# Kernel optimization log

Measured on AMD Instinct MI355X. Metric: run time of the kernel, lower is better.

Reference implementation:

```python
import jax, jax.numpy as jnp
import numpy as np
from jax import lax

B, T, D, U = 128, 1024, 256, 48


def setup_inputs() -> dict:
    key = jax.random.key(0)
    k1, k2, k3 = jax.random.split(key, 3)
    x = jax.random.normal(k1, (B, T, D), dtype=jnp.float32)
    kernel = jax.random.normal(k2, (D, U), dtype=jnp.float32) * (1.0 / np.sqrt(D))
    bias = jnp.zeros((U,), dtype=jnp.float32)
    chain_kernel = jax.random.normal(k3, (U, U), dtype=jnp.float32)
    return {"x": x, "kernel": kernel, "bias": bias, "chain_kernel": chain_kernel}


def _viterbi_decode(logits, trans):
    # logits: [B, T, U], trans: [U, U]; full-length sequences (mask=None)
    init_state = logits[:, 0]  # [B, U]
    steps = jnp.swapaxes(logits[:, 1:], 0, 1)  # [T-1, B, U]

    def fwd(state, logit_t):
        # scores[b, i, j] = state[b, i] + trans[i, j]
        scores = state[:, :, None] + trans[None]  # [B, U, U]
        bp = jnp.argmax(scores, axis=1)            # [B, U] best prev tag
        new_state = logit_t + jnp.max(scores, axis=1)
        return new_state, bp

    final_state, bps = lax.scan(fwd, init_state, steps)  # bps: [T-1, B, U]
    last_tag = jnp.argmax(final_state, axis=-1)          # [B]

    def back(tag, bp):
        prev = jnp.take_along_axis(bp, tag[:, None], axis=1)[:, 0]
        return prev, prev

    # reverse scan emits tags for t = 0..T-2 in forward time order
    _, tags_head = lax.scan(back, last_tag, bps, reverse=True)  # [T-1, B]
    tags = jnp.concatenate([tags_head, last_tag[None]], axis=0)  # [T, B]
    return jnp.transpose(tags)  # [B, T]


def reference(x, kernel, bias, chain_kernel):
    # _dense_layer: linear activation -> x @ kernel + bias
    logits = jnp.einsum('btd,du->btu', x, kernel) + bias  # [B, T, U]
    pred_ids = _viterbi_decode(logits, chain_kernel)       # [B, T] int
    return pred_ids.astype(jnp.float32)
```

## Files before the change

kernel.cpp:

```cpp
#include <hip/hip_runtime.h>
#include <cstdint>

#define B_ 128
#define T_ 1024
#define D_ 256
#define U_ 48

__device__ __forceinline__ float max3f(float a, float b, float c) {
    float d;
    asm("v_max3_f32 %0, %1, %2, %3" : "=v"(d) : "v"(a), "v"(b), "v"(c));
    return d;
}

__global__ __launch_bounds__(256, 1) void k_logits(const float* __restrict__ x,
                                                   const float* __restrict__ kern,
                                                   const float* __restrict__ bias,
                                                   float* __restrict__ logits) {
    __shared__ float K[D_ * U_];
    __shared__ float bsh[U_];
    const int tid = threadIdx.x;
    for (int i = tid; i < D_ * U_; i += 256) K[i] = kern[i];
    if (tid < U_) bsh[tid] = bias[tid];
    __syncthreads();

    const long row0 = (long)blockIdx.x * 256 + tid;
    const long row1 = row0 + (long)B_ * T_ / 2;
    const float4* xr0 = (const float4*)(x + row0 * D_);
    const float4* xr1 = (const float4*)(x + row1 * D_);

    float a0[U_], a1[U_];
#pragma unroll
    for (int u = 0; u < U_; ++u) { a0[u] = 0.0f; a1[u] = 0.0f; }

#pragma unroll 1
    for (int blk = 0; blk < D_ / 32; ++blk) {
        float4 xa[8], xb[8];
#pragma unroll
        for (int i = 0; i < 8; ++i) xa[i] = xr0[blk * 8 + i];
#pragma unroll
        for (int i = 0; i < 8; ++i) xb[i] = xr1[blk * 8 + i];

#pragma unroll
        for (int i = 0; i < 8; ++i) {
            const int d4 = blk * 8 + i;
            const float xc0[4] = {xa[i].x, xa[i].y, xa[i].z, xa[i].w};
            const float xc1[4] = {xb[i].x, xb[i].y, xb[i].z, xb[i].w};
#pragma unroll
            for (int c = 0; c < 4; ++c) {
                const float4* kp = (const float4*)&K[(d4 * 4 + c) * U_];
                const float s0 = xc0[c], s1 = xc1[c];
#pragma unroll
                for (int u4 = 0; u4 < U_ / 4; ++u4) {
                    float4 kv = kp[u4];
                    a0[u4*4+0] += s0 * kv.x;  a1[u4*4+0] += s1 * kv.x;
                    a0[u4*4+1] += s0 * kv.y;  a1[u4*4+1] += s1 * kv.y;
                    a0[u4*4+2] += s0 * kv.z;  a1[u4*4+2] += s1 * kv.z;
                    a0[u4*4+3] += s0 * kv.w;  a1[u4*4+3] += s1 * kv.w;
                }
            }
        }
    }

    float4* o0 = (float4*)(logits + row0 * U_);
    float4* o1 = (float4*)(logits + row1 * U_);
#pragma unroll
    for (int i = 0; i < U_ / 4; ++i) {
        float4 v0, v1;
        v0.x = a0[i*4+0] + bsh[i*4+0];  v1.x = a1[i*4+0] + bsh[i*4+0];
        v0.y = a0[i*4+1] + bsh[i*4+1];  v1.y = a1[i*4+1] + bsh[i*4+1];
        v0.z = a0[i*4+2] + bsh[i*4+2];  v1.z = a1[i*4+2] + bsh[i*4+2];
        v0.w = a0[i*4+3] + bsh[i*4+3];  v1.w = a1[i*4+3] + bsh[i*4+3];
        o0[i] = v0;
        o1[i] = v1;
    }
}

__device__ __forceinline__ float maxplus_rlb(float state, const float* tc) {
    const int si = __float_as_int(state);
    int sv[U_];
#pragma unroll
    for (int v = 0; v < U_; ++v) sv[v] = __builtin_amdgcn_readlane(si, v);
    __builtin_amdgcn_sched_barrier(0);
    float cf[U_];
#pragma unroll
    for (int v = 0; v < U_; ++v) cf[v] = __int_as_float(sv[v]) + tc[v];
    float t1[16];
#pragma unroll
    for (int i = 0; i < 16; ++i) t1[i] = max3f(cf[3*i], cf[3*i+1], cf[3*i+2]);
    float t2[6];
#pragma unroll
    for (int i = 0; i < 5; ++i) t2[i] = max3f(t1[3*i], t1[3*i+1], t1[3*i+2]);
    t2[5] = t1[15];
    return fmaxf(max3f(t2[0], t2[1], t2[2]), max3f(t2[3], t2[4], t2[5]));
}

__global__ __launch_bounds__(64, 1) void k_forward(const float* __restrict__ trans,
                                                   const float* __restrict__ logits,
                                                   float* __restrict__ delta) {
    const int lane = threadIdx.x;
    const int b = blockIdx.x;
    const int u = (lane < U_) ? lane : (U_ - 1);

    float tc[U_];
#pragma unroll
    for (int v = 0; v < U_; ++v) tc[v] = trans[v * U_ + u];

    const float* lin = logits + (long)b * T_ * U_;
    float* dout = delta + (long)b * T_ * U_;

    float state = lin[u];
    dout[u] = state;

    float pf[8];
#pragma unroll
    for (int i = 0; i < 8; ++i) pf[i] = lin[(1 + i) * U_ + u];

    const float* lp = lin + 9 * U_ + u;
    float* dp = dout + 1 * U_ + u;

#pragma unroll 1
    for (int g = 0; g < 127; ++g) {
#pragma unroll
        for (int j = 0; j < 8; ++j) {
            const float logit = pf[j];
            pf[j] = lp[j * U_];
            const float m = maxplus_rlb(state, tc);
            state = logit + m;
            dp[j * U_] = state;
        }
        lp += 8 * U_;
        dp += 8 * U_;
    }

#pragma unroll
    for (int j = 0; j < 7; ++j) {
        const float m = maxplus_rlb(state, tc);
        state = pf[j] + m;
        dp[j * U_] = state;
    }
}

__global__ __launch_bounds__(64, 1) void k_forward_inplace(const float* __restrict__ trans,
                                                           float* __restrict__ delta) {
    const int lane = threadIdx.x;
    const int b = blockIdx.x;
    const int u = (lane < U_) ? lane : (U_ - 1);

    float tc[U_];
#pragma unroll
    for (int v = 0; v < U_; ++v) tc[v] = trans[v * U_ + u];

    float* base = delta + (long)b * T_ * U_;
    float state = base[u];

#pragma unroll 1
    for (int t = 1; t < T_; ++t) {
        const float logit = base[(long)t * U_ + u];
        const float m = maxplus_rlb(state, tc);
        state = logit + m;
        base[(long)t * U_ + u] = state;
    }
}

#define BP_ROWS 32
__global__ __launch_bounds__(64, 1) void k_bp(const float* __restrict__ trans,
                                              const float* __restrict__ delta,
                                              unsigned char* __restrict__ bp) {
    __shared__ float sbuf[2][U_];
    const int lane = threadIdx.x;
    const int u = (lane < U_) ? lane : (U_ - 1);

    float tc[U_];
#pragma unroll
    for (int v = 0; v < U_; ++v) tc[v] = trans[v * U_ + u];

    const int NROW = B_ * (T_ - 1);
    const int row0 = blockIdx.x * BP_ROWS;
    if (row0 >= NROW) return;

    int b = row0 / (T_ - 1);
    int tm1 = row0 - b * (T_ - 1);

    float dval = delta[((long)b * T_ + tm1) * U_ + u];

#pragma unroll 1
    for (int i = 0; i < BP_ROWS; ++i) {
        const int row = row0 + i;
        if (row >= NROW) break;

        sbuf[i & 1][u] = dval;

        int bn = b, tn = tm1 + 1;
        if (tn == T_ - 1) { tn = 0; bn = b + 1; }
        float dnext = 0.0f;
        if (row + 1 < NROW) dnext = delta[((long)bn * T_ + tn) * U_ + u];

        const float4* sb4 = (const float4*)sbuf[i & 1];
        float best = -3.4e38f;
        int bi = 0;
#pragma unroll
        for (int k = 0; k < U_ / 4; ++k) {
            float4 s = sb4[k];
            float c0 = s.x + tc[4*k+0];
            float c1 = s.y + tc[4*k+1];
            float c2 = s.z + tc[4*k+2];
            float c3 = s.w + tc[4*k+3];
            bi = (c0 > best) ? 4*k+0 : bi;  best = fmaxf(best, c0);
            bi = (c1 > best) ? 4*k+1 : bi;  best = fmaxf(best, c1);
            bi = (c2 > best) ? 4*k+2 : bi;  best = fmaxf(best, c2);
            bi = (c3 > best) ? 4*k+3 : bi;  best = fmaxf(best, c3);
        }
        bp[(long)row * U_ + u] = (unsigned char)bi;

        b = bn; tm1 = tn; dval = dnext;
    }
}

__global__ __launch_bounds__(64) void k_back(const float* __restrict__ delta,
                                             const unsigned char* __restrict__ bp,
                                             float* __restrict__ out) {
    __shared__ unsigned char bpl[(T_ - 1) * U_];
    __shared__ float tags[T_];
    __shared__ float fin[U_];
    const int lane = threadIdx.x;
    const int b = blockIdx.x;

    const uint32_t* src = (const uint32_t*)(bp + (long)b * (T_ - 1) * U_);
    uint32_t* dst = (uint32_t*)bpl;
    const int NW = (T_ - 1) * U_ / 4;
    for (int i = lane; i < NW; i += 64) dst[i] = src[i];
    if (lane < U_) fin[lane] = delta[((long)b * T_ + (T_ - 1)) * U_ + lane];
    __syncthreads();

    if (lane == 0) {
        float best = fin[0];
        int tag = 0;
        for (int uu = 1; uu < U_; ++uu)
            if (fin[uu] > best) { best = fin[uu]; tag = uu; }
        tags[T_ - 1] = (float)tag;
        for (int t = T_ - 1; t >= 1; --t) {
            tag = bpl[(t - 1) * U_ + tag];
            tags[t - 1] = (float)tag;
        }
    }
    __syncthreads();

    float* o = out + (long)b * T_;
    for (int i = lane; i < T_; i += 64) o[i] = tags[i];
}

extern "C" void kernel_launch(void* const* d_in, const int* in_sizes, int n_in,
                              void* d_out, int out_size, void* d_ws, size_t ws_size,
                              hipStream_t stream) {
    const float* x     = (const float*)d_in[0];
    const float* kern  = (const float*)d_in[1];
    const float* bias  = (const float*)d_in[2];
    const float* trans = (const float*)d_in[3];
    float* out = (float*)d_out;

    const size_t NBT = (size_t)B_ * T_ * U_ * sizeof(float);

    float* logits = (float*)d_ws;
    const bool two_buf = ws_size >= 2 * NBT + (size_t)B_ * T_ * U_;
    float* delta = two_buf ? (float*)((char*)d_ws + NBT) : logits;
    unsigned char* bp = (unsigned char*)d_ws + (two_buf ? 2 * NBT : NBT);

    const int NROW = B_ * (T_ - 1);
    const int bp_grid = (NROW + BP_ROWS - 1) / BP_ROWS;

    k_logits<<<(B_ * T_ / 2) / 256, 256, 0, stream>>>(x, kern, bias, logits);
    if (two_buf)
        k_forward<<<B_, 64, 0, stream>>>(trans, logits, delta);
    else
        k_forward_inplace<<<B_, 64, 0, stream>>>(trans, logits);
    k_bp  <<<bp_grid, 64, 0, stream>>>(trans, delta, bp);
    k_back<<<B_,      64, 0, stream>>>(delta, bp, out);
}
```

Baseline: 565.9 us.

## Replace readlane broadcast with DPP wave rotation in Viterbi max-plus step

```diff
diff --git a/kernel.cpp b/kernel.cpp
--- a/kernel.cpp
+++ b/kernel.cpp
@@ -10,6 +10,10 @@
     float d;
     asm("v_max3_f32 %0, %1, %2, %3" : "=v"(d) : "v"(a), "v"(b), "v"(c));
     return d;
+}
+
+__device__ __forceinline__ float ror1f(float x) {
+    return __int_as_float(__builtin_amdgcn_mov_dpp(__float_as_int(x), 0x13C, 0xF, 0xF, true));
 }
 
 __global__ __launch_bounds__(256, 1) void k_logits(const float* __restrict__ x,
@@ -75,23 +79,45 @@
     }
 }
 
-__device__ __forceinline__ float maxplus_rlb(float state, const float* tc) {
-    const int si = __float_as_int(state);
-    int sv[U_];
-#pragma unroll
-    for (int v = 0; v < U_; ++v) sv[v] = __builtin_amdgcn_readlane(si, v);
-    __builtin_amdgcn_sched_barrier(0);
-    float cf[U_];
-#pragma unroll
-    for (int v = 0; v < U_; ++v) cf[v] = __int_as_float(sv[v]) + tc[v];
-    float t1[16];
-#pragma unroll
-    for (int i = 0; i < 16; ++i) t1[i] = max3f(cf[3*i], cf[3*i+1], cf[3*i+2]);
-    float t2[6];
-#pragma unroll
-    for (int i = 0; i < 5; ++i) t2[i] = max3f(t1[3*i], t1[3*i+1], t1[3*i+2]);
-    t2[5] = t1[15];
-    return fmaxf(max3f(t2[0], t2[1], t2[2]), max3f(t2[3], t2[4], t2[5]));
+__device__ __forceinline__ float maxplus_dpp(float state, const float* tr,
+                                             int lane, int baddr) {
+    const float rsrc = (lane < U_) ? state : -3.0e38f;
+    const int rbi = __builtin_amdgcn_ds_bpermute(baddr, __float_as_int(rsrc));
+
+    float rA = rsrc;
+    float c0 = rA + tr[0];
+    rA = ror1f(rA);
+    float c1 = rA + tr[1];
+    float m = fmaxf(c0, c1);
+#pragma unroll
+    for (int k = 2; k < 32; k += 2) {
+        rA = ror1f(rA); float ca = rA + tr[k];
+        rA = ror1f(rA); float cb = rA + tr[k + 1];
+        m = max3f(m, ca, cb);
+    }
+    float rB = __int_as_float(rbi);
+    float d0 = rB + tr[32];
+    rB = ror1f(rB);
+    float d1 = rB + tr[33];
+    m = max3f(m, d0, d1);
+#pragma unroll
+    for (int k = 34; k < 64; k += 2) {
+        rB = ror1f(rB); float ca = rB + tr[k];
+        rB = ror1f(rB); float cb = rB + tr[k + 1];
+        m = max3f(m, ca, cb);
+    }
+    return m;
+}
+
+__device__ __forceinline__ void load_tr(const float* __restrict__ trans,
+                                        float* tr, int lane, int u) {
+    const int p = __builtin_amdgcn_mov_dpp(lane, 0x13C, 0xF, 0xF, true);
+    const int dirm = (p - lane) & 63;
+#pragma unroll
+    for (int k = 0; k < 64; ++k) {
+        const int w = (lane + dirm * k) & 63;
+        tr[k] = (w < U_) ? trans[w * U_ + u] : 0.0f;
+    }
 }
 
 __global__ __launch_bounds__(64, 1) void k_forward(const float* __restrict__ trans,
@@ -100,16 +126,16 @@
     const int lane = threadIdx.x;
     const int b = blockIdx.x;
     const int u = (lane < U_) ? lane : (U_ - 1);
-
-    float tc[U_];
-#pragma unroll
-    for (int v = 0; v < U_; ++v) tc[v] = trans[v * U_ + u];
+    const int baddr = ((lane + 32) & 63) * 4;
+
+    float tr[64];
+    load_tr(trans, tr, lane, u);
 
     const float* lin = logits + (long)b * T_ * U_;
     float* dout = delta + (long)b * T_ * U_;
 
     float state = lin[u];
-    dout[u] = state;
+    if (lane < U_) dout[u] = state;
 
     float pf[8];
 #pragma unroll
@@ -124,9 +150,9 @@
         for (int j = 0; j < 8; ++j) {
             const float logit = pf[j];
             pf[j] = lp[j * U_];
-            const float m = maxplus_rlb(state, tc);
+            const float m = maxplus_dpp(state, tr, lane, baddr);
             state = logit + m;
-            dp[j * U_] = state;
+            if (lane < U_) dp[j * U_] = state;
         }
         lp += 8 * U_;
         dp += 8 * U_;
@@ -134,9 +160,9 @@
 
 #pragma unroll
     for (int j = 0; j < 7; ++j) {
-        const float m = maxplus_rlb(state, tc);
+        const float m = maxplus_dpp(state, tr, lane, baddr);
         state = pf[j] + m;
-        dp[j * U_] = state;
+        if (lane < U_) dp[j * U_] = state;
     }
 }
 
@@ -145,10 +171,10 @@
     const int lane = threadIdx.x;
     const int b = blockIdx.x;
     const int u = (lane < U_) ? lane : (U_ - 1);
-
-    float tc[U_];
-#pragma unroll
-    for (int v = 0; v < U_; ++v) tc[v] = trans[v * U_ + u];
+    const int baddr = ((lane + 32) & 63) * 4;
+
+    float tr[64];
+    load_tr(trans, tr, lane, u);
 
     float* base = delta + (long)b * T_ * U_;
     float state = base[u];
@@ -156,9 +182,9 @@
 #pragma unroll 1
     for (int t = 1; t < T_; ++t) {
         const float logit = base[(long)t * U_ + u];
-        const float m = maxplus_rlb(state, tc);
+        const float m = maxplus_dpp(state, tr, lane, baddr);
         state = logit + m;
-        base[(long)t * U_ + u] = state;
+        if (lane < U_) base[(long)t * U_ + u] = state;
     }
 }
 
```

Result: slower. 737.9 us (+30.4%).
